# Optimization experiments

Measured on AMD Instinct MI355X. Metric: run time of the kernel, lower is better.

The kernel has to match this reference:

```python
import jax, jax.numpy as jnp
import numpy as np

OUT_FEATURES = 4096
IN_FEATURES = 4096
RANK = 64
ALPHA = 1.0
SCALING = ALPHA / float(RANK)  # w1 direct, w2 factored -> effective_alpha = alpha


def setup_inputs() -> dict:
    key = jax.random.key(0)
    k_x, k_w1, k_a, k_b = jax.random.split(key, 4)
    x = jax.random.normal(k_x, (4, 2048, IN_FEATURES), dtype=jnp.float32)
    lokr_w1 = jax.random.normal(k_w1, (8, 8), dtype=jnp.float32)        # [out_l, in_m]
    lokr_w2_a = jax.random.normal(k_a, (512, RANK), dtype=jnp.float32)  # [out_k, rank]
    lokr_w2_b = jax.random.normal(k_b, (RANK, 512), dtype=jnp.float32)  # [rank, in_n]
    return {"x": x, "lokr_w1": lokr_w1, "lokr_w2_a": lokr_w2_a, "lokr_w2_b": lokr_w2_b}


def reference(x, lokr_w1, lokr_w2_a, lokr_w2_b):
    # w2 = w2_a @ w2_b : [out_k, in_n]
    w2 = lokr_w2_a @ lokr_w2_b
    # kron(w1, w2): element (i*out_k + k, j*in_n + l) = w1[i,j] * w2[k,l]
    out_l, in_m = lokr_w1.shape
    out_k, in_n = w2.shape
    diff = jnp.einsum('ij,kl->ikjl', lokr_w1, w2).reshape(out_l * out_k, in_m * in_n)
    diff = diff * SCALING  # [out_features, in_features]
    # F.linear(x, diff) = x @ diff.T
    return jnp.einsum('bsi,oi->bso', x, diff)
```

## Files before the change

### kernel.cpp

```cpp
#include <hip/hip_runtime.h>
#include <hip/hip_bf16.h>


typedef __attribute__((ext_vector_type(4))) float f32x4;
typedef __attribute__((ext_vector_type(8))) short s16x8;
typedef __attribute__((ext_vector_type(4))) short s16x4;

__device__ inline unsigned short f2bf(float f) {
    unsigned u = __float_as_uint(f);
    u += 0x7FFF + ((u >> 16) & 1);
    return (unsigned short)(u >> 16);
}

__global__ void lokr_pre(const float* __restrict__ w1,
                         const float* __restrict__ a,
                         const float* __restrict__ b,
                         unsigned short* __restrict__ b_bf,
                         unsigned short* __restrict__ a_bf,
                         float* __restrict__ w1s) {
    int i = blockIdx.x * 256 + threadIdx.x;
    if (i < 32768) {
        b_bf[i] = f2bf(b[i]);
        a_bf[i] = f2bf(a[i]);
    }
    if (i < 64) w1s[i] = w1[i] * (1.0f / 64.0f);
}

#define LSTR 72

__global__ __launch_bounds__(256, 4) void lokr_main(
    const float* __restrict__ x,
    const unsigned short* __restrict__ b_bf,
    const unsigned short* __restrict__ a_bf,
    const float* __restrict__ w1s,
    float* __restrict__ out)
{
    __shared__ __attribute__((aligned(16))) unsigned short xs[2][128 * LSTR];
    __shared__ __attribute__((aligned(16))) unsigned short vs[128 * LSTR];
    __shared__ float w1_s[64];

    const int t    = threadIdx.x;
    const int wave = t >> 6;
    const int lane = t & 63;
    const int col  = lane & 15;
    const int quad = lane >> 4;
    const long rowbase = (long)blockIdx.x * 128;

    if (t < 64) w1_s[t] = w1s[t];

    const int lrow = t >> 4;
    const int lcol = (t & 15) * 4;

    float4 xb[8];
    {
        const float* xg = x + (rowbase + lrow) * 512 + lcol;
        #pragma unroll
        for (int i = 0; i < 8; ++i)
            xb[i] = *(const float4*)(xg + (long)i * 16 * 512);
    }
    #pragma unroll
    for (int i = 0; i < 8; ++i) {
        s16x4 h;
        h[0] = (short)f2bf(xb[i].x); h[1] = (short)f2bf(xb[i].y);
        h[2] = (short)f2bf(xb[i].z); h[3] = (short)f2bf(xb[i].w);
        *(s16x4*)&xs[0][(lrow + i * 16) * LSTR + lcol] = h;
    }
    __syncthreads();

    f32x4 acc[8];
    #pragma unroll
    for (int m = 0; m < 8; ++m) acc[m] = (f32x4){0.f, 0.f, 0.f, 0.f};

    const unsigned short* brow = b_bf + (wave * 16 + col) * 512 + quad * 8;

    #pragma unroll 2
    for (int s = 0; s < 8; ++s) {
        s16x8 bf0 = *(const s16x8*)(brow + s * 64);
        s16x8 bf1 = *(const s16x8*)(brow + s * 64 + 32);
        if (s < 7) {
            const float* xg = x + (rowbase + lrow) * 512 + (s + 1) * 64 + lcol;
            #pragma unroll
            for (int i = 0; i < 8; ++i)
                xb[i] = *(const float4*)(xg + (long)i * 16 * 512);
        }
        const unsigned short* xa = &xs[s & 1][col * LSTR + quad * 8];
        #pragma unroll
        for (int m = 0; m < 8; ++m) {
            s16x8 a0 = *(const s16x8*)(xa + m * 16 * LSTR);
            s16x8 a1 = *(const s16x8*)(xa + m * 16 * LSTR + 32);
            acc[m] = __builtin_amdgcn_mfma_f32_16x16x32_bf16(a0, bf0, acc[m], 0, 0, 0);
            acc[m] = __builtin_amdgcn_mfma_f32_16x16x32_bf16(a1, bf1, acc[m], 0, 0, 0);
        }
        if (s < 7) {
            #pragma unroll
            for (int i = 0; i < 8; ++i) {
                s16x4 h;
                h[0] = (short)f2bf(xb[i].x); h[1] = (short)f2bf(xb[i].y);
                h[2] = (short)f2bf(xb[i].z); h[3] = (short)f2bf(xb[i].w);
                *(s16x4*)&xs[(s + 1) & 1][(lrow + i * 16) * LSTR + lcol] = h;
            }
        }
        __syncthreads();
    }

    #pragma unroll
    for (int m = 0; m < 8; ++m) {
        float own[4], oth[4], tij[8];
        #pragma unroll
        for (int j = 0; j < 4; ++j) own[j] = acc[m][j];
        #pragma unroll
        for (int j = 0; j < 4; ++j) oth[j] = __shfl_xor(own[j], 16);
        if ((quad & 1) == 0) {
            #pragma unroll
            for (int j = 0; j < 4; ++j) { tij[j] = own[j]; tij[4 + j] = oth[j]; }
        } else {
            #pragma unroll
            for (int j = 0; j < 4; ++j) { tij[j] = oth[j]; tij[4 + j] = own[j]; }
        }
        const int plocal = m * 2 + (quad >> 1);
        const int oib = (quad & 1) * 4;
        #pragma unroll
        for (int oo = 0; oo < 4; ++oo) {
            float v = 0.f;
            #pragma unroll
            for (int j = 0; j < 8; ++j) v += w1_s[(oib + oo) * 8 + j] * tij[j];
            vs[(plocal * 8 + oib + oo) * LSTR + wave * 16 + col] = f2bf(v);
        }
    }
    __syncthreads();

    s16x8 va0[8], va1[8];
    #pragma unroll
    for (int m = 0; m < 8; ++m) {
        const unsigned short* vp = &vs[(m * 16 + col) * LSTR + quad * 8];
        va0[m] = *(const s16x8*)(vp);
        va1[m] = *(const s16x8*)(vp + 32);
    }

    const unsigned short* ab = a_bf + (wave * 128 + col) * 64 + quad * 8;
    float* ob = out + (long)blockIdx.x * 65536 + wave * 128 + col;

    for (int nt = 0; nt < 8; ++nt) {
        s16x8 af0 = *(const s16x8*)(ab + nt * 16 * 64);
        s16x8 af1 = *(const s16x8*)(ab + nt * 16 * 64 + 32);
        #pragma unroll
        for (int m = 0; m < 8; ++m) {
            f32x4 c = {0.f, 0.f, 0.f, 0.f};
            c = __builtin_amdgcn_mfma_f32_16x16x32_bf16(va0[m], af0, c, 0, 0, 0);
            c = __builtin_amdgcn_mfma_f32_16x16x32_bf16(va1[m], af1, c, 0, 0, 0);
            #pragma unroll
            for (int reg = 0; reg < 4; ++reg) {
                const int rl = m * 16 + quad * 4 + reg;
                ob[(long)rl * 512 + nt * 16] = c[reg];
            }
        }
    }
}

extern "C" void kernel_launch(void* const* d_in, const int* in_sizes, int n_in,
                              void* d_out, int out_size, void* d_ws, size_t ws_size,
                              hipStream_t stream) {
    const float* x  = (const float*)d_in[0];
    const float* w1 = (const float*)d_in[1];
    const float* a  = (const float*)d_in[2];
    const float* b  = (const float*)d_in[3];

    unsigned short* b_bf = (unsigned short*)d_ws;
    unsigned short* a_bf = b_bf + 32768;
    float*          w1s  = (float*)(a_bf + 32768);

    lokr_pre<<<128, 256, 0, stream>>>(w1, a, b, b_bf, a_bf, w1s);
    lokr_main<<<512, 256, 0, stream>>>(x, b_bf, a_bf, w1s, (float*)d_out);
}
```

Measured before the change: 268.0 us.

## Halve row tile, alias V buffer onto X buffer, vectorize output stores via swapped MFMA

Each block now handles 64 rows instead of 128, doubling the grid to 1024 blocks, and the V staging buffer reuses the X double-buffer in shared memory to cut LDS use. The second GEMM swaps its MFMA operands so each lane holds four consecutive output columns and writes them as one 16-byte store, replacing scattered scalar stores. B and A fragments are prefetched one iteration ahead in registers, and the final barrier of the first loop is skipped. The intent is more occupancy and coalesced output writes, at the cost of less reuse of B and A fragments per block.

```diff
diff --git a/kernel.cpp b/kernel.cpp
--- a/kernel.cpp
+++ b/kernel.cpp
@@ -35,31 +35,31 @@
     const float* __restrict__ w1s,
     float* __restrict__ out)
 {
-    __shared__ __attribute__((aligned(16))) unsigned short xs[2][128 * LSTR];
-    __shared__ __attribute__((aligned(16))) unsigned short vs[128 * LSTR];
+    __shared__ __attribute__((aligned(16))) unsigned short xs[2][64 * LSTR];
     __shared__ float w1_s[64];
+    unsigned short* vs = &xs[0][0];
 
     const int t    = threadIdx.x;
     const int wave = t >> 6;
     const int lane = t & 63;
     const int col  = lane & 15;
     const int quad = lane >> 4;
-    const long rowbase = (long)blockIdx.x * 128;
+    const long rowbase = (long)blockIdx.x * 64;
 
     if (t < 64) w1_s[t] = w1s[t];
 
     const int lrow = t >> 4;
     const int lcol = (t & 15) * 4;
 
-    float4 xb[8];
+    float4 xb[4];
     {
         const float* xg = x + (rowbase + lrow) * 512 + lcol;
         #pragma unroll
-        for (int i = 0; i < 8; ++i)
+        for (int i = 0; i < 4; ++i)
             xb[i] = *(const float4*)(xg + (long)i * 16 * 512);
     }
     #pragma unroll
-    for (int i = 0; i < 8; ++i) {
+    for (int i = 0; i < 4; ++i) {
         s16x4 h;
         h[0] = (short)f2bf(xb[i].x); h[1] = (short)f2bf(xb[i].y);
         h[2] = (short)f2bf(xb[i].z); h[3] = (short)f2bf(xb[i].w);
@@ -67,44 +67,48 @@
     }
     __syncthreads();
 
-    f32x4 acc[8];
+    f32x4 acc[4];
     #pragma unroll
-    for (int m = 0; m < 8; ++m) acc[m] = (f32x4){0.f, 0.f, 0.f, 0.f};
+    for (int m = 0; m < 4; ++m) acc[m] = (f32x4){0.f, 0.f, 0.f, 0.f};
 
     const unsigned short* brow = b_bf + (wave * 16 + col) * 512 + quad * 8;
+    s16x8 bc0 = *(const s16x8*)(brow);
+    s16x8 bc1 = *(const s16x8*)(brow + 32);
 
     #pragma unroll 2
     for (int s = 0; s < 8; ++s) {
-        s16x8 bf0 = *(const s16x8*)(brow + s * 64);
-        s16x8 bf1 = *(const s16x8*)(brow + s * 64 + 32);
+        s16x8 bn0, bn1;
         if (s < 7) {
+            bn0 = *(const s16x8*)(brow + (s + 1) * 64);
+            bn1 = *(const s16x8*)(brow + (s + 1) * 64 + 32);
             const float* xg = x + (rowbase + lrow) * 512 + (s + 1) * 64 + lcol;
             #pragma unroll
-            for (int i = 0; i < 8; ++i)
+            for (int i = 0; i < 4; ++i)
                 xb[i] = *(const float4*)(xg + (long)i * 16 * 512);
         }
         const unsigned short* xa = &xs[s & 1][col * LSTR + quad * 8];
         #pragma unroll
-        for (int m = 0; m < 8; ++m) {
+        for (int m = 0; m < 4; ++m) {
             s16x8 a0 = *(const s16x8*)(xa + m * 16 * LSTR);
             s16x8 a1 = *(const s16x8*)(xa + m * 16 * LSTR + 32);
-            acc[m] = __builtin_amdgcn_mfma_f32_16x16x32_bf16(a0, bf0, acc[m], 0, 0, 0);
-            acc[m] = __builtin_amdgcn_mfma_f32_16x16x32_bf16(a1, bf1, acc[m], 0, 0, 0);
+            acc[m] = __builtin_amdgcn_mfma_f32_16x16x32_bf16(a0, bc0, acc[m], 0, 0, 0);
+            acc[m] = __builtin_amdgcn_mfma_f32_16x16x32_bf16(a1, bc1, acc[m], 0, 0, 0);
         }
         if (s < 7) {
             #pragma unroll
-            for (int i = 0; i < 8; ++i) {
+            for (int i = 0; i < 4; ++i) {
                 s16x4 h;
                 h[0] = (short)f2bf(xb[i].x); h[1] = (short)f2bf(xb[i].y);
                 h[2] = (short)f2bf(xb[i].z); h[3] = (short)f2bf(xb[i].w);
                 *(s16x4*)&xs[(s + 1) & 1][(lrow + i * 16) * LSTR + lcol] = h;
             }
+            __syncthreads();
+            bc0 = bn0; bc1 = bn1;
         }
-        __syncthreads();
     }
 
     #pragma unroll
-    for (int m = 0; m < 8; ++m) {
+    for (int m = 0; m < 4; ++m) {
         float own[4], oth[4], tij[8];
         #pragma unroll
         for (int j = 0; j < 4; ++j) own[j] = acc[m][j];
@@ -129,31 +133,34 @@
     }
     __syncthreads();
 
-    s16x8 va0[8], va1[8];
+    s16x8 va0[4], va1[4];
     #pragma unroll
-    for (int m = 0; m < 8; ++m) {
+    for (int m = 0; m < 4; ++m) {
         const unsigned short* vp = &vs[(m * 16 + col) * LSTR + quad * 8];
         va0[m] = *(const s16x8*)(vp);
         va1[m] = *(const s16x8*)(vp + 32);
     }
 
     const unsigned short* ab = a_bf + (wave * 128 + col) * 64 + quad * 8;
-    float* ob = out + (long)blockIdx.x * 65536 + wave * 128 + col;
+    s16x8 ac0 = *(const s16x8*)(ab);
+    s16x8 ac1 = *(const s16x8*)(ab + 32);
+
+    float* ob = out + (rowbase + col) * 512 + wave * 128 + quad * 4;
 
     for (int nt = 0; nt < 8; ++nt) {
-        s16x8 af0 = *(const s16x8*)(ab + nt * 16 * 64);
-        s16x8 af1 = *(const s16x8*)(ab + nt * 16 * 64 + 32);
+        s16x8 an0, an1;
+        if (nt < 7) {
+            an0 = *(const s16x8*)(ab + (nt + 1) * 1024);
+            an1 = *(const s16x8*)(ab + (nt + 1) * 1024 + 32);
+        }
         #pragma unroll
-        for (int m = 0; m < 8; ++m) {
+        for (int m = 0; m < 4; ++m) {
             f32x4 c = {0.f, 0.f, 0.f, 0.f};
-            c = __builtin_amdgcn_mfma_f32_16x16x32_bf16(va0[m], af0, c, 0, 0, 0);
-            c = __builtin_amdgcn_mfma_f32_16x16x32_bf16(va1[m], af1, c, 0, 0, 0);
-            #pragma unroll
-            for (int reg = 0; reg < 4; ++reg) {
-                const int rl = m * 16 + quad * 4 + reg;
-                ob[(long)rl * 512 + nt * 16] = c[reg];
-            }
+            c = __builtin_amdgcn_mfma_f32_16x16x32_bf16(ac0, va0[m], c, 0, 0, 0);
+            c = __builtin_amdgcn_mfma_f32_16x16x32_bf16(ac1, va1[m], c, 0, 0, 0);
+            *(f32x4*)(ob + (long)m * 16 * 512 + nt * 16) = c;
         }
+        if (nt < 7) { ac0 = an0; ac1 = an1; }
     }
 }
 
@@ -170,5 +177,5 @@
     float*          w1s  = (float*)(a_bf + 32768);
 
     lokr_pre<<<128, 256, 0, stream>>>(w1, a, b, b_bf, a_bf, w1s);
-    lokr_main<<<512, 256, 0, stream>>>(x, b_bf, a_bf, w1s, (float*)d_out);
+    lokr_main<<<1024, 256, 0, stream>>>(x, b_bf, a_bf, w1s, (float*)d_out);
 }
```

New measurement: 256.9 us. 1.04x faster.
